# Performance work log

Measured on AMD Instinct MI355X. Metric: run time of the kernel, lower is better.

Reference implementation:

```python
import jax, jax.numpy as jnp
import numpy as np

T, HID, H, KV, D = 2048, 2048, 16, 8, 128
EPS = 1e-6
THETA = 10000.0


def setup_inputs() -> dict:
    key = jax.random.key(0)
    ks = jax.random.split(key, 6)
    positions = jnp.arange(T, dtype=jnp.int64 if jax.config.jax_enable_x64 else jnp.int32)
    hidden_states = jax.random.normal(ks[0], (T, HID), dtype=jnp.float32)
    scale = 0.02
    Wq = jax.random.normal(ks[1], (HID, H * 2 * D), dtype=jnp.float32) * scale
    Wk = jax.random.normal(ks[2], (HID, KV * D), dtype=jnp.float32) * scale
    Wv = jax.random.normal(ks[3], (HID, KV * D), dtype=jnp.float32) * scale
    Wo = jax.random.normal(ks[4], (H * D, HID), dtype=jnp.float32) * scale
    q_norm_w = jnp.zeros((D,), dtype=jnp.float32)  # torch init: zeros, applied as (1+w)
    k_norm_w = jnp.zeros((D,), dtype=jnp.float32)
    return {"positions": positions, "hidden_states": hidden_states, "Wq": Wq,
            "Wk": Wk, "Wv": Wv, "Wo": Wo, "q_norm_w": q_norm_w, "k_norm_w": k_norm_w}


def _rms_norm(x, w):
    # fp32 RMSNorm with (1 + weight) scaling, per last dim
    xf = x.astype(jnp.float32)
    inv = jax.lax.rsqrt(jnp.mean(xf * xf, axis=-1, keepdims=True) + EPS)
    return (xf * inv * (1.0 + w.astype(jnp.float32))).astype(x.dtype)


def _rope(x, positions):
    # neox-style rotary over full head_dim; x: (T, heads, D)
    half = D // 2
    inv_freq = 1.0 / (THETA ** (jnp.arange(0, half, dtype=jnp.float32) / half))
    freqs = positions.astype(jnp.float32)[:, None] * inv_freq  # (T, half)
    cos = jnp.cos(freqs)[:, None, :]  # (T,1,half)
    sin = jnp.sin(freqs)[:, None, :]
    x1, x2 = x[..., :half], x[..., half:]
    return jnp.concatenate([x1 * cos - x2 * sin, x2 * cos + x1 * sin], axis=-1)


def reference(positions, hidden_states, Wq, Wk, Wv, Wo, q_norm_w, k_norm_w):
    scaling = D ** -0.5
    qg = (hidden_states @ Wq).reshape(T, H, 2 * D)
    q, gate = qg[..., :D], qg[..., D:]              # (T,H,D) each
    k = (hidden_states @ Wk).reshape(T, KV, D)
    v = (hidden_states @ Wv).reshape(T, KV, D)
    q = _rms_norm(q, q_norm_w)
    k = _rms_norm(k, k_norm_w)
    q = _rope(q, positions)
    k = _rope(k, positions)
    # GQA: repeat kv heads
    rep = H // KV
    k = jnp.repeat(k, rep, axis=1)                   # (T,H,D)
    v = jnp.repeat(v, rep, axis=1)
    scores = jnp.einsum('thd,shd->hts', q, k) * scaling  # (H,T,T)
    causal = positions[:, None] >= positions[None, :]     # (T,T)
    scores = jnp.where(causal[None], scores, jnp.finfo(scores.dtype).min)
    probs = jax.nn.softmax(scores, axis=-1)
    o = jnp.einsum('hts,shd->thd', probs, v).reshape(T, H * D)
    o = o * jax.nn.sigmoid(gate.reshape(T, H * D))
    return o @ Wo
```

## Files before the change

kernel.cpp:

```cpp
#include <hip/hip_runtime.h>
#include <stdint.h>
#include <math.h>

#define T_SEQ 2048
#define HID   2048
#define NH    16
#define NKV   8
#define DH    128

typedef __bf16 bf16x8 __attribute__((ext_vector_type(8)));
typedef float  f32x4  __attribute__((ext_vector_type(4)));

__device__ __forceinline__ ushort f2bf(float f) {
  uint32_t u = __float_as_uint(f);
  u += 0x7FFF + ((u >> 16) & 1);
  return (ushort)(u >> 16);
}
__device__ __forceinline__ ushort f2bf_rz(float f) {
  return (ushort)(__float_as_uint(f) >> 16);
}
__device__ __forceinline__ float bf2f(ushort u) {
  return __uint_as_float(((uint32_t)u) << 16);
}
__device__ __forceinline__ void gld16(const void* g, void* l) {
  __builtin_amdgcn_global_load_lds(
      (const __attribute__((address_space(1))) uint32_t*)g,
      (__attribute__((address_space(3))) uint32_t*)l, 16, 0, 0);
}

__global__ __launch_bounds__(256) void prep_kernel(
    const float* __restrict__ hs, const float* __restrict__ Wq,
    const float* __restrict__ Wk, const float* __restrict__ Wv,
    const float* __restrict__ Wo, ushort* __restrict__ hs16,
    ushort* __restrict__ Wqt, ushort* __restrict__ Wkt,
    ushort* __restrict__ Wvt, ushort* __restrict__ Wot) {
  int bid = blockIdx.x;
  if (bid < 4096) {
    int i = (bid * 256 + threadIdx.x) * 4;
    float4 v = *(const float4*)(hs + i);
    ushort4 o = {f2bf(v.x), f2bf(v.y), f2bf(v.z), f2bf(v.w)};
    *(ushort4*)(hs16 + i) = o;
    return;
  }
  bid -= 4096;
  const float* src; ushort* dst; int N, bi, bj;
  if (bid < 2048)      { src = Wq; dst = Wqt; N = 4096; bj = bid & 63; bi = bid >> 6; }
  else if (bid < 2560) { bid -= 2048; src = Wk; dst = Wkt; N = 1024; bj = bid & 15; bi = bid >> 4; }
  else if (bid < 3072) { bid -= 2560; src = Wv; dst = Wvt; N = 1024; bj = bid & 15; bi = bid >> 4; }
  else                 { bid -= 3072; src = Wo; dst = Wot; N = 2048; bj = bid & 31; bi = bid >> 5; }
  __shared__ float tile[64][65];
  const int r = threadIdx.x >> 2, cg = (threadIdx.x & 3) * 16;
  const float* sp = src + (size_t)(bi * 64 + r) * N + bj * 64 + cg;
#pragma unroll
  for (int p = 0; p < 4; ++p) {
    float4 v = *(const float4*)(sp + p * 4);
    tile[r][cg + p * 4 + 0] = v.x; tile[r][cg + p * 4 + 1] = v.y;
    tile[r][cg + p * 4 + 2] = v.z; tile[r][cg + p * 4 + 3] = v.w;
  }
  __syncthreads();
  ushort* dp = dst + (size_t)(bj * 64 + r) * HID + bi * 64 + cg;
#pragma unroll
  for (int p = 0; p < 2; ++p) {
    union { uint4 v; ushort u[8]; } o;
#pragma unroll
    for (int j = 0; j < 8; ++j) o.u[j] = f2bf(tile[cg + p * 8 + j][r]);
    *(uint4*)(dp + p * 8) = o.v;
  }
}

template <int MI>
__device__ __forceinline__ void gemm_loop(
    const ushort* __restrict__ A, const ushort* __restrict__ Bt,
    int K, int m0, int n0, ushort* As, ushort* Bs, f32x4 (*acc)[4]) {
  const int tid = threadIdx.x, lane = tid & 63, w = tid >> 6;
  const int quad = lane >> 4, l15 = lane & 15;
  const int wm = (w >> 1) * (MI * 16), wn = (w & 1) * 64;
  const int srow = tid >> 2, sch = tid & 3;
  for (int k0 = 0; k0 < K; k0 += 32) {
    __syncthreads();
#pragma unroll
    for (int p = 0; p < MI / 2; ++p) {
      int row = p * 64 + srow;
      int gch = sch ^ ((row >> 1) & 3);
      gld16(A + (size_t)(m0 + row) * K + k0 + gch * 8,
            As + (p * 256 + w * 64) * 8);
    }
#pragma unroll
    for (int p = 0; p < 2; ++p) {
      int row = p * 64 + srow;
      int gch = sch ^ ((row >> 1) & 3);
      gld16(Bt + (size_t)(n0 + row) * K + k0 + gch * 8,
            Bs + (p * 256 + w * 64) * 8);
    }
    __syncthreads();
    bf16x8 af[MI], bfr[4];
#pragma unroll
    for (int mi = 0; mi < MI; ++mi) {
      int row = wm + mi * 16 + l15;
      int pch = quad ^ ((row >> 1) & 3);
      af[mi] = *(const bf16x8*)(As + row * 32 + pch * 8);
    }
#pragma unroll
    for (int ni = 0; ni < 4; ++ni) {
      int row = wn + ni * 16 + l15;
      int pch = quad ^ ((row >> 1) & 3);
      bfr[ni] = *(const bf16x8*)(Bs + row * 32 + pch * 8);
    }
#pragma unroll
    for (int mi = 0; mi < MI; ++mi)
#pragma unroll
      for (int ni = 0; ni < 4; ++ni)
        acc[mi][ni] = __builtin_amdgcn_mfma_f32_16x16x32_bf16(
            af[mi], bfr[ni], acc[mi][ni], 0, 0, 0);
  }
}

__device__ __forceinline__ void bf16_store(f32x4 (*acc)[4],
                                           ushort* __restrict__ Cb, int Ncols,
                                           int m0, int n0) {
  const int lane = threadIdx.x & 63, w = threadIdx.x >> 6;
  const int quad = lane >> 4, l15 = lane & 15;
  const int wm = (w >> 1) * 64, wn = (w & 1) * 64;
#pragma unroll
  for (int mi = 0; mi < 4; ++mi)
#pragma unroll
    for (int ni = 0; ni < 4; ++ni)
#pragma unroll
      for (int r = 0; r < 4; ++r) {
        int row = m0 + wm + mi * 16 + quad * 4 + r;
        int col = n0 + wn + ni * 16 + l15;
        Cb[(size_t)row * Ncols + col] = f2bf(acc[mi][ni][r]);
      }
}

__global__ __launch_bounds__(256) void gemm_qkv(
    const ushort* __restrict__ hs16, const ushort* __restrict__ Wqt,
    const ushort* __restrict__ Wkt, const ushort* __restrict__ Wvt,
    ushort* __restrict__ q16, ushort* __restrict__ gate16,
    ushort* __restrict__ k16, ushort* __restrict__ v16t) {
  __shared__ ushort As[128 * 32];
  __shared__ ushort Bs[128 * 32];
  f32x4 acc[4][4];
#pragma unroll
  for (int i = 0; i < 4; ++i)
#pragma unroll
    for (int j = 0; j < 4; ++j) acc[i][j] = (f32x4){0.f, 0.f, 0.f, 0.f};
  const int b = blockIdx.x;
  if (b < 512) {
    int mt = b >> 5, nt = b & 31, m0 = mt * 128;
    gemm_loop<4>(hs16, Wqt, HID, m0, nt * 128, As, Bs, acc);
    ushort* dst = ((nt & 1) == 0) ? q16 : gate16;
    bf16_store(acc, dst, NH * DH, m0, (nt >> 1) * 128);
  } else if (b < 640) {
    int f = b - 512, m0 = (f >> 3) * 128, n0 = (f & 7) * 128;
    gemm_loop<4>(hs16, Wkt, HID, m0, n0, As, Bs, acc);
    bf16_store(acc, k16, 1024, m0, n0);
  } else {
    int f = b - 640, m0 = (f >> 4) * 128, n0 = (f & 15) * 128;
    gemm_loop<4>(Wvt, hs16, HID, m0, n0, As, Bs, acc);
    bf16_store(acc, v16t, T_SEQ, m0, n0);
  }
}

__global__ __launch_bounds__(256) void gemm_out(
    const ushort* __restrict__ ob16, const ushort* __restrict__ Wot,
    float* __restrict__ out) {
  __shared__ ushort As[64 * 32];
  __shared__ ushort Bs[128 * 32];
  f32x4 acc[2][4];
#pragma unroll
  for (int i = 0; i < 2; ++i)
#pragma unroll
    for (int j = 0; j < 4; ++j) acc[i][j] = (f32x4){0.f, 0.f, 0.f, 0.f};
  const int b = blockIdx.x;
  const int m0 = (b >> 4) * 64, n0 = (b & 15) * 128;
  gemm_loop<2>(ob16, Wot, HID, m0, n0, As, Bs, acc);
  const int lane = threadIdx.x & 63, w = threadIdx.x >> 6;
  const int quad = lane >> 4, l15 = lane & 15;
  const int wm = (w >> 1) * 32, wn = (w & 1) * 64;
#pragma unroll
  for (int mi = 0; mi < 2; ++mi)
#pragma unroll
    for (int ni = 0; ni < 4; ++ni)
#pragma unroll
      for (int r = 0; r < 4; ++r) {
        int row = m0 + wm + mi * 16 + quad * 4 + r;
        int col = n0 + wn + ni * 16 + l15;
        out[(size_t)row * HID + col] = acc[mi][ni][r];
      }
}

__global__ __launch_bounds__(256) void norm_rope_fast(
    ushort* __restrict__ q16, ushort* __restrict__ k16,
    const int* __restrict__ positions, const float* __restrict__ qw,
    const float* __restrict__ kw) {
  const int tid = threadIdx.x, lg = tid & 15;
  const int r = blockIdx.x * 16 + (tid >> 4);
  ushort* x; const float* wgt; int t;
  if (r < T_SEQ * NH) { t = r >> 4; x = q16 + (size_t)r * DH; wgt = qw; }
  else { int rr = r - T_SEQ * NH; t = rr >> 3; x = k16 + (size_t)rr * DH; wgt = kw; }

  ushort* xp = x + lg * 8;
  ushort4 a = *(const ushort4*)(xp);
  ushort4 bq = *(const ushort4*)(xp + 4);
  float xv[8] = {bf2f(a.x), bf2f(a.y), bf2f(a.z), bf2f(a.w),
                 bf2f(bq.x), bf2f(bq.y), bf2f(bq.z), bf2f(bq.w)};

  float ss = 0.f;
#pragma unroll
  for (int j = 0; j < 8; ++j) ss += xv[j] * xv[j];
  ss += __shfl_xor(ss, 1, 16);
  ss += __shfl_xor(ss, 2, 16);
  ss += __shfl_xor(ss, 4, 16);
  ss += __shfl_xor(ss, 8, 16);
  const float rstd = rsqrtf(ss * (1.f / 128.f) + 1e-6f);

  const int dbase = lg * 8;
  float xn[8];
#pragma unroll
  for (int j = 0; j < 8; ++j) xn[j] = xv[j] * rstd * (1.f + wgt[dbase + j]);

  float pr[8];
#pragma unroll
  for (int j = 0; j < 8; ++j) pr[j] = __shfl_xor(xn[j], 8, 16);

  const float pos = (float)positions[t];
  const int dh = dbase & 63;
  const bool lo = (lg < 8);
  ushort o[8];
#pragma unroll
  for (int j = 0; j < 8; ++j) {
    float rev = pos * exp2f((float)(dh + j) * -0.20762050593045233f) *
                0.15915494309189535f;
    float fr = rev - floorf(rev);
    float s = __builtin_amdgcn_sinf(fr);
    float c = __builtin_amdgcn_cosf(fr);
    float out = lo ? (xn[j] * c - pr[j] * s) : (xn[j] * c + pr[j] * s);
    o[j] = f2bf(out);
  }
  *(ushort4*)(xp)     = (ushort4){o[0], o[1], o[2], o[3]};
  *(ushort4*)(xp + 4) = (ushort4){o[4], o[5], o[6], o[7]};
}

__device__ __forceinline__ void stage_kv(const ushort* __restrict__ k16,
                                         const ushort* __restrict__ v16t,
                                         int kvh, int kt0, ushort* Ksb,
                                         ushort* Vsb, int tid) {
  const int w = tid >> 6;
#pragma unroll
  for (int p = 0; p < 4; ++p) {
    int row = p * 16 + (tid >> 4), ch = tid & 15;
    int gch = ch ^ (row & 15);
    gld16(k16 + ((size_t)(kt0 + row) * NKV + kvh) * DH + gch * 8,
          Ksb + (p * 256 + w * 64) * 8);
  }
#pragma unroll
  for (int p = 0; p < 4; ++p) {
    int row = p * 32 + (tid >> 3), ch = tid & 7;
    int gch = ch ^ (row & 7);
    gld16(v16t + (size_t)(kvh * DH + row) * T_SEQ + kt0 + gch * 8,
          Vsb + (p * 256 + w * 64) * 8);
  }
}

__global__ __launch_bounds__(256) void attn_mfma(
    const ushort* __restrict__ q16, const ushort* __restrict__ k16,
    const ushort* __restrict__ v16t, const float* __restrict__ qnw,
    const float* __restrict__ knw, ushort* __restrict__ Op0,
    ushort* __restrict__ Op1, float* __restrict__ lpart) {
  const int pb = blockIdx.x, h = blockIdx.y, s = blockIdx.z, kvh = h >> 1;
  const int tid = threadIdx.x, lane = tid & 63, w = tid >> 6;
  const int quad = lane >> 4, l15 = lane & 15;

  __shared__ ushort Ks[2][64 * 128];
  __shared__ ushort Vs[2][128 * 64];
  __shared__ ushort Ones[16 * 64];
  __shared__ ushort Ps[4][16][72];

  for (int i = tid; i < 16 * 64; i += 256)
    Ones[i] = (i < 64) ? (ushort)0x3F80 : (ushort)0;

  __shared__ float s8[8];
  __shared__ float bshare;
  {
    float mq = 0.f, mk = 0.f;
    if (tid < 128) { mq = fabsf(1.f + qnw[tid]); mk = fabsf(1.f + knw[tid]); }
#pragma unroll
    for (int off = 32; off >= 1; off >>= 1) {
      mq = fmaxf(mq, __shfl_xor(mq, off, 64));
      mk = fmaxf(mk, __shfl_xor(mk, off, 64));
    }
    if (lane == 0) { s8[w * 2] = mq; s8[w * 2 + 1] = mk; }
    __syncthreads();
    if (tid == 0) {
      float MQ = fmaxf(s8[0], s8[2]), MK = fmaxf(s8[1], s8[3]);
      bshare = 16.3217f * MQ * MK * 1.02f + 0.1f;
    }
    __syncthreads();
  }
  const float B = bshare;
  const float CSC = 0.08838834764831845f * 1.44269504088896f;

#pragma unroll 1
  for (int sel = 0; sel < 2; ++sel) {
    const int qt = sel ? (31 - pb) : pb;
    const int q0 = qt * 64;
    const int ntl = (qt >= s) ? ((qt - s) / 2 + 1) : 0;

    bf16x8 qf[4];
    const ushort* qbase = q16 + ((size_t)(q0 + w * 16 + l15) * NH + h) * DH;
#pragma unroll
    for (int ks = 0; ks < 4; ++ks)
      qf[ks] = *(const bf16x8*)(qbase + ks * 32 + quad * 8);

    f32x4 oacc[9];
#pragma unroll
    for (int i = 0; i < 9; ++i) oacc[i] = (f32x4){0.f, 0.f, 0.f, 0.f};

    if (ntl > 0) stage_kv(k16, v16t, kvh, s * 64, Ks[0], Vs[0], tid);

#pragma unroll 1
    for (int it = 0; it < ntl; ++it) {
      const int kt = s + 2 * it;
      const int kt0 = kt * 64;
      const int cur = it & 1;
      if (it + 1 < ntl) {
        stage_kv(k16, v16t, kvh, (kt + 2) * 64, Ks[cur ^ 1], Vs[cur ^ 1], tid);
        asm volatile("s_waitcnt vmcnt(8)" ::: "memory");
      } else {
        asm volatile("s_waitcnt vmcnt(0)" ::: "memory");
      }
      asm volatile("s_barrier" ::: "memory");

      f32x4 sacc[4];
#pragma unroll
      for (int ni = 0; ni < 4; ++ni) sacc[ni] = (f32x4){0.f, 0.f, 0.f, 0.f};
#pragma unroll
      for (int ks = 0; ks < 4; ++ks)
#pragma unroll
        for (int ni = 0; ni < 4; ++ni) {
          int row = ni * 16 + l15;
          int pch = (ks * 4 + quad) ^ (row & 15);
          bf16x8 kf = *(const bf16x8*)(&Ks[cur][row * 128 + pch * 8]);
          sacc[ni] = __builtin_amdgcn_mfma_f32_16x16x32_bf16(
              qf[ks], kf, sacc[ni], 0, 0, 0);
        }

      const bool diag = (kt == qt);
#pragma unroll
      for (int ni = 0; ni < 4; ++ni) {
        int key = kt0 + ni * 16 + l15;
#pragma unroll
        for (int r = 0; r < 4; ++r) {
          float arg = fmaf(sacc[ni][r], CSC, -B);
          float pv;
          if (diag) {
            int q = q0 + w * 16 + quad * 4 + r;
            pv = (key <= q) ? exp2f(arg) : 0.f;
          } else {
            pv = exp2f(arg);
          }
          Ps[w][quad * 4 + r][ni * 16 + l15] = f2bf_rz(pv);
        }
      }

#pragma unroll
      for (int ks2 = 0; ks2 < 2; ++ks2) {
        bf16x8 pf = *(const bf16x8*)(&Ps[w][l15][ks2 * 32 + quad * 8]);
#pragma unroll
        for (int ni = 0; ni < 9; ++ni) {
          int row = ni * 16 + l15;
          int pch = (ks2 * 4 + quad) ^ (row & 7);
          const ushort* vp = (ni < 8) ? &Vs[cur][row * 64 + pch * 8]
                                      : &Ones[l15 * 64 + pch * 8];
          bf16x8 vf = *(const bf16x8*)(vp);
          oacc[ni] = __builtin_amdgcn_mfma_f32_16x16x32_bf16(
              pf, vf, oacc[ni], 0, 0, 0);
        }
      }
      asm volatile("s_barrier" ::: "memory");
    }

    ushort* Op = s ? Op1 : Op0;
#pragma unroll
    for (int ni = 0; ni < 8; ++ni) {
      int d = ni * 16 + l15;
#pragma unroll
      for (int r = 0; r < 4; ++r) {
        int q = q0 + w * 16 + quad * 4 + r;
        Op[((size_t)h * T_SEQ + q) * DH + d] = f2bf(oacc[ni][r]);
      }
    }
    if (l15 == 0) {
#pragma unroll
      for (int r = 0; r < 4; ++r) {
        int q = q0 + w * 16 + quad * 4 + r;
        lpart[(size_t)s * (NH * T_SEQ) + h * T_SEQ + q] = oacc[8][r];
      }
    }
  }
}

__global__ __launch_bounds__(256) void combine_kernel(
    const ushort* __restrict__ Op0, const ushort* __restrict__ Op1,
    const float* __restrict__ lpart, const ushort* __restrict__ gate16,
    ushort* __restrict__ ob16) {
  const int t = blockIdx.x, tid = threadIdx.x;
  const int h = tid >> 4, d0 = (tid & 15) * 8;
  const int NT = NH * T_SEQ;
  const float l = lpart[h * T_SEQ + t] + lpart[NT + h * T_SEQ + t];
  const float inv = 1.0f / l;
  const size_t po = ((size_t)h * T_SEQ + t) * DH + d0;
  ushort4 a0 = *(const ushort4*)(Op0 + po);
  ushort4 a1 = *(const ushort4*)(Op0 + po + 4);
  ushort4 b0 = *(const ushort4*)(Op1 + po);
  ushort4 b1 = *(const ushort4*)(Op1 + po + 4);
  const ushort* gp = gate16 + (size_t)t * (NH * DH) + h * DH + d0;
  ushort4 g0 = *(const ushort4*)(gp);
  ushort4 g1 = *(const ushort4*)(gp + 4);
  float oa[8] = {bf2f(a0.x), bf2f(a0.y), bf2f(a0.z), bf2f(a0.w),
                 bf2f(a1.x), bf2f(a1.y), bf2f(a1.z), bf2f(a1.w)};
  float ob[8] = {bf2f(b0.x), bf2f(b0.y), bf2f(b0.z), bf2f(b0.w),
                 bf2f(b1.x), bf2f(b1.y), bf2f(b1.z), bf2f(b1.w)};
  float gg[8] = {bf2f(g0.x), bf2f(g0.y), bf2f(g0.z), bf2f(g0.w),
                 bf2f(g1.x), bf2f(g1.y), bf2f(g1.z), bf2f(g1.w)};
  ushort r[8];
#pragma unroll
  for (int i = 0; i < 8; ++i) {
    float o = (oa[i] + ob[i]) * inv;
    o = o / (1.0f + exp2f(-gg[i] * 1.44269504088896f));
    r[i] = f2bf(o);
  }
  ushort* op = ob16 + (size_t)t * (NH * DH) + h * DH + d0;
  *(ushort4*)(op)     = (ushort4){r[0], r[1], r[2], r[3]};
  *(ushort4*)(op + 4) = (ushort4){r[4], r[5], r[6], r[7]};
}

extern "C" void kernel_launch(void* const* d_in, const int* in_sizes, int n_in,
                              void* d_out, int out_size, void* d_ws, size_t ws_size,
                              hipStream_t stream) {
  const int*   positions = (const int*)d_in[0];
  const float* hs  = (const float*)d_in[1];
  const float* Wq  = (const float*)d_in[2];
  const float* Wk  = (const float*)d_in[3];
  const float* Wv  = (const float*)d_in[4];
  const float* Wo  = (const float*)d_in[5];
  const float* qnw = (const float*)d_in[6];
  const float* knw = (const float*)d_in[7];
  float* out = (float*)d_out;

  const size_t MB = 1 << 20;
  uint8_t* ws = (uint8_t*)d_ws;
  ushort* hs16  = (ushort*)(ws + 0);
  ushort* Op0   = (ushort*)(ws + 0);
  ushort* Wqt   = (ushort*)(ws + 8 * MB);
  ushort* Op1   = (ushort*)(ws + 8 * MB);
  ushort* Wkt   = (ushort*)(ws + 24 * MB);
  ushort* ob16  = (ushort*)(ws + 24 * MB);
  ushort* Wvt   = (ushort*)(ws + 28 * MB);
  ushort* v16t  = (ushort*)(ws + 32 * MB);
  ushort* k16   = (ushort*)(ws + 36 * MB);
  ushort* q16   = (ushort*)(ws + 40 * MB);
  ushort* gate16= (ushort*)(ws + 48 * MB);
  ushort* Wot   = (ushort*)(ws + 56 * MB);
  float*  lpart = (float*)d_out;

  prep_kernel<<<8192, 256, 0, stream>>>(hs, Wq, Wk, Wv, Wo,
                                        hs16, Wqt, Wkt, Wvt, Wot);
  gemm_qkv<<<768, 256, 0, stream>>>(hs16, Wqt, Wkt, Wvt,
                                    q16, gate16, k16, v16t);
  norm_rope_fast<<<3072, 256, 0, stream>>>(q16, k16, positions, qnw, knw);
  attn_mfma<<<dim3(16, NH, 2), 256, 0, stream>>>(q16, k16, v16t, qnw, knw,
                                                 Op0, Op1, lpart);
  combine_kernel<<<T_SEQ, 256, 0, stream>>>(Op0, Op1, lpart, gate16, ob16);
  gemm_out<<<512, 256, 0, stream>>>(ob16, Wot, out);
}
```

Baseline: 272.4 us.

## Fuse attention combine into attn kernel; split-K output GEMM with atomics

Attention no longer splits the key range into two partial passes. Each block now processes every causal key tile for its query tiles and applies normalisation and the sigmoid gate directly in its epilogue, which removes the combine kernel and the partial-output round trip through memory. The output projection switches to 128x128 tiles with a 2-way K split and accumulates into a pre-zeroed output using float atomics, keeping the grid at 512 blocks. The cost is half as many attention blocks, so less parallelism there, plus an extra zeroing kernel, atomic traffic, and a summation order that is no longer deterministic.

Result: slower. 312.2 us (+14.6%).

```diff
diff --git a/kernel.cpp b/kernel.cpp
--- a/kernel.cpp
+++ b/kernel.cpp
@@ -26,6 +26,11 @@
   __builtin_amdgcn_global_load_lds(
       (const __attribute__((address_space(1))) uint32_t*)g,
       (__attribute__((address_space(3))) uint32_t*)l, 16, 0, 0);
+}
+
+__global__ __launch_bounds__(256) void zero_out(float* __restrict__ out) {
+  int i = (blockIdx.x * 256 + threadIdx.x) * 4;
+  *(float4*)(out + i) = (float4){0.f, 0.f, 0.f, 0.f};
 }
 
 __global__ __launch_bounds__(256) void prep_kernel(
@@ -71,25 +76,26 @@
 template <int MI>
 __device__ __forceinline__ void gemm_loop(
     const ushort* __restrict__ A, const ushort* __restrict__ Bt,
-    int K, int m0, int n0, ushort* As, ushort* Bs, f32x4 (*acc)[4]) {
+    int ld, int kbeg, int kend, int m0, int n0, ushort* As, ushort* Bs,
+    f32x4 (*acc)[4]) {
   const int tid = threadIdx.x, lane = tid & 63, w = tid >> 6;
   const int quad = lane >> 4, l15 = lane & 15;
   const int wm = (w >> 1) * (MI * 16), wn = (w & 1) * 64;
   const int srow = tid >> 2, sch = tid & 3;
-  for (int k0 = 0; k0 < K; k0 += 32) {
+  for (int k0 = kbeg; k0 < kend; k0 += 32) {
     __syncthreads();
 #pragma unroll
     for (int p = 0; p < MI / 2; ++p) {
       int row = p * 64 + srow;
       int gch = sch ^ ((row >> 1) & 3);
-      gld16(A + (size_t)(m0 + row) * K + k0 + gch * 8,
+      gld16(A + (size_t)(m0 + row) * ld + k0 + gch * 8,
             As + (p * 256 + w * 64) * 8);
     }
 #pragma unroll
     for (int p = 0; p < 2; ++p) {
       int row = p * 64 + srow;
       int gch = sch ^ ((row >> 1) & 3);
-      gld16(Bt + (size_t)(n0 + row) * K + k0 + gch * 8,
+      gld16(Bt + (size_t)(n0 + row) * ld + k0 + gch * 8,
             Bs + (p * 256 + w * 64) * 8);
     }
     __syncthreads();
@@ -148,16 +154,16 @@
   const int b = blockIdx.x;
   if (b < 512) {
     int mt = b >> 5, nt = b & 31, m0 = mt * 128;
-    gemm_loop<4>(hs16, Wqt, HID, m0, nt * 128, As, Bs, acc);
+    gemm_loop<4>(hs16, Wqt, HID, 0, HID, m0, nt * 128, As, Bs, acc);
     ushort* dst = ((nt & 1) == 0) ? q16 : gate16;
     bf16_store(acc, dst, NH * DH, m0, (nt >> 1) * 128);
   } else if (b < 640) {
     int f = b - 512, m0 = (f >> 3) * 128, n0 = (f & 7) * 128;
-    gemm_loop<4>(hs16, Wkt, HID, m0, n0, As, Bs, acc);
+    gemm_loop<4>(hs16, Wkt, HID, 0, HID, m0, n0, As, Bs, acc);
     bf16_store(acc, k16, 1024, m0, n0);
   } else {
     int f = b - 640, m0 = (f >> 4) * 128, n0 = (f & 15) * 128;
-    gemm_loop<4>(Wvt, hs16, HID, m0, n0, As, Bs, acc);
+    gemm_loop<4>(Wvt, hs16, HID, 0, HID, m0, n0, As, Bs, acc);
     bf16_store(acc, v16t, T_SEQ, m0, n0);
   }
 }
@@ -165,28 +171,32 @@
 __global__ __launch_bounds__(256) void gemm_out(
     const ushort* __restrict__ ob16, const ushort* __restrict__ Wot,
     float* __restrict__ out) {
-  __shared__ ushort As[64 * 32];
+  __shared__ ushort As[128 * 32];
   __shared__ ushort Bs[128 * 32];
-  f32x4 acc[2][4];
-#pragma unroll
-  for (int i = 0; i < 2; ++i)
+  f32x4 acc[4][4];
+#pragma unroll
+  for (int i = 0; i < 4; ++i)
 #pragma unroll
     for (int j = 0; j < 4; ++j) acc[i][j] = (f32x4){0.f, 0.f, 0.f, 0.f};
   const int b = blockIdx.x;
-  const int m0 = (b >> 4) * 64, n0 = (b & 15) * 128;
-  gemm_loop<2>(ob16, Wot, HID, m0, n0, As, Bs, acc);
+  const int tilei = b & 255, ks = b >> 8;
+  const int m0 = (tilei >> 4) * 128, n0 = (tilei & 15) * 128;
+  const int kbeg = ks * (HID / 2);
+  gemm_loop<4>(ob16, Wot, HID, kbeg, kbeg + HID / 2, m0, n0, As, Bs, acc);
   const int lane = threadIdx.x & 63, w = threadIdx.x >> 6;
   const int quad = lane >> 4, l15 = lane & 15;
-  const int wm = (w >> 1) * 32, wn = (w & 1) * 64;
-#pragma unroll
-  for (int mi = 0; mi < 2; ++mi)
+  const int wm = (w >> 1) * 64, wn = (w & 1) * 64;
+#pragma unroll
+  for (int mi = 0; mi < 4; ++mi)
 #pragma unroll
     for (int ni = 0; ni < 4; ++ni)
 #pragma unroll
       for (int r = 0; r < 4; ++r) {
         int row = m0 + wm + mi * 16 + quad * 4 + r;
         int col = n0 + wn + ni * 16 + l15;
-        out[(size_t)row * HID + col] = acc[mi][ni][r];
+        __hip_atomic_fetch_add(&out[(size_t)row * HID + col],
+                               acc[mi][ni][r], __ATOMIC_RELAXED,
+                               __HIP_MEMORY_SCOPE_AGENT);
       }
 }
 
@@ -266,9 +276,9 @@
 __global__ __launch_bounds__(256) void attn_mfma(
     const ushort* __restrict__ q16, const ushort* __restrict__ k16,
     const ushort* __restrict__ v16t, const float* __restrict__ qnw,
-    const float* __restrict__ knw, ushort* __restrict__ Op0,
-    ushort* __restrict__ Op1, float* __restrict__ lpart) {
-  const int pb = blockIdx.x, h = blockIdx.y, s = blockIdx.z, kvh = h >> 1;
+    const float* __restrict__ knw, const ushort* __restrict__ gate16,
+    ushort* __restrict__ ob16) {
+  const int pb = blockIdx.x, h = blockIdx.y, kvh = h >> 1;
   const int tid = threadIdx.x, lane = tid & 63, w = tid >> 6;
   const int quad = lane >> 4, l15 = lane & 15;
 
@@ -305,7 +315,7 @@
   for (int sel = 0; sel < 2; ++sel) {
     const int qt = sel ? (31 - pb) : pb;
     const int q0 = qt * 64;
-    const int ntl = (qt >= s) ? ((qt - s) / 2 + 1) : 0;
+    const int ntl = qt + 1;
 
     bf16x8 qf[4];
     const ushort* qbase = q16 + ((size_t)(q0 + w * 16 + l15) * NH + h) * DH;
@@ -317,15 +327,14 @@
 #pragma unroll
     for (int i = 0; i < 9; ++i) oacc[i] = (f32x4){0.f, 0.f, 0.f, 0.f};
 
-    if (ntl > 0) stage_kv(k16, v16t, kvh, s * 64, Ks[0], Vs[0], tid);
+    stage_kv(k16, v16t, kvh, 0, Ks[0], Vs[0], tid);
 
 #pragma unroll 1
     for (int it = 0; it < ntl; ++it) {
-      const int kt = s + 2 * it;
-      const int kt0 = kt * 64;
+      const int kt0 = it * 64;
       const int cur = it & 1;
       if (it + 1 < ntl) {
-        stage_kv(k16, v16t, kvh, (kt + 2) * 64, Ks[cur ^ 1], Vs[cur ^ 1], tid);
+        stage_kv(k16, v16t, kvh, (it + 1) * 64, Ks[cur ^ 1], Vs[cur ^ 1], tid);
         asm volatile("s_waitcnt vmcnt(8)" ::: "memory");
       } else {
         asm volatile("s_waitcnt vmcnt(0)" ::: "memory");
@@ -346,7 +355,7 @@
               qf[ks], kf, sacc[ni], 0, 0, 0);
         }
 
-      const bool diag = (kt == qt);
+      const bool diag = (it == qt);
 #pragma unroll
       for (int ni = 0; ni < 4; ++ni) {
         int key = kt0 + ni * 16 + l15;
@@ -381,59 +390,23 @@
       asm volatile("s_barrier" ::: "memory");
     }
 
-    ushort* Op = s ? Op1 : Op0;
-#pragma unroll
-    for (int ni = 0; ni < 8; ++ni) {
-      int d = ni * 16 + l15;
-#pragma unroll
-      for (int r = 0; r < 4; ++r) {
-        int q = q0 + w * 16 + quad * 4 + r;
-        Op[((size_t)h * T_SEQ + q) * DH + d] = f2bf(oacc[ni][r]);
-      }
-    }
-    if (l15 == 0) {
-#pragma unroll
-      for (int r = 0; r < 4; ++r) {
-        int q = q0 + w * 16 + quad * 4 + r;
-        lpart[(size_t)s * (NH * T_SEQ) + h * T_SEQ + q] = oacc[8][r];
-      }
-    }
-  }
-}
-
-__global__ __launch_bounds__(256) void combine_kernel(
-    const ushort* __restrict__ Op0, const ushort* __restrict__ Op1,
-    const float* __restrict__ lpart, const ushort* __restrict__ gate16,
-    ushort* __restrict__ ob16) {
-  const int t = blockIdx.x, tid = threadIdx.x;
-  const int h = tid >> 4, d0 = (tid & 15) * 8;
-  const int NT = NH * T_SEQ;
-  const float l = lpart[h * T_SEQ + t] + lpart[NT + h * T_SEQ + t];
-  const float inv = 1.0f / l;
-  const size_t po = ((size_t)h * T_SEQ + t) * DH + d0;
-  ushort4 a0 = *(const ushort4*)(Op0 + po);
-  ushort4 a1 = *(const ushort4*)(Op0 + po + 4);
-  ushort4 b0 = *(const ushort4*)(Op1 + po);
-  ushort4 b1 = *(const ushort4*)(Op1 + po + 4);
-  const ushort* gp = gate16 + (size_t)t * (NH * DH) + h * DH + d0;
-  ushort4 g0 = *(const ushort4*)(gp);
-  ushort4 g1 = *(const ushort4*)(gp + 4);
-  float oa[8] = {bf2f(a0.x), bf2f(a0.y), bf2f(a0.z), bf2f(a0.w),
-                 bf2f(a1.x), bf2f(a1.y), bf2f(a1.z), bf2f(a1.w)};
-  float ob[8] = {bf2f(b0.x), bf2f(b0.y), bf2f(b0.z), bf2f(b0.w),
-                 bf2f(b1.x), bf2f(b1.y), bf2f(b1.z), bf2f(b1.w)};
-  float gg[8] = {bf2f(g0.x), bf2f(g0.y), bf2f(g0.z), bf2f(g0.w),
-                 bf2f(g1.x), bf2f(g1.y), bf2f(g1.z), bf2f(g1.w)};
-  ushort r[8];
-#pragma unroll
-  for (int i = 0; i < 8; ++i) {
-    float o = (oa[i] + ob[i]) * inv;
-    o = o / (1.0f + exp2f(-gg[i] * 1.44269504088896f));
-    r[i] = f2bf(o);
-  }
-  ushort* op = ob16 + (size_t)t * (NH * DH) + h * DH + d0;
-  *(ushort4*)(op)     = (ushort4){r[0], r[1], r[2], r[3]};
-  *(ushort4*)(op + 4) = (ushort4){r[4], r[5], r[6], r[7]};
+#pragma unroll
+    for (int r = 0; r < 4; ++r) {
+      float l = __shfl(oacc[8][r], quad << 4, 64);
+      float inv = 1.0f / l;
+      const int q = q0 + w * 16 + quad * 4 + r;
+      const ushort* gp = gate16 + (size_t)q * (NH * DH) + h * DH;
+      ushort* op = ob16 + (size_t)q * (NH * DH) + h * DH;
+#pragma unroll
+      for (int ni = 0; ni < 8; ++ni) {
+        int d = ni * 16 + l15;
+        float g = bf2f(gp[d]);
+        float o = oacc[ni][r] * inv;
+        o = o / (1.0f + exp2f(-g * 1.44269504088896f));
+        op[d] = f2bf(o);
+      }
+    }
+  }
 }
 
 extern "C" void kernel_launch(void* const* d_in, const int* in_sizes, int n_in,
@@ -452,9 +425,7 @@
   const size_t MB = 1 << 20;
   uint8_t* ws = (uint8_t*)d_ws;
   ushort* hs16  = (ushort*)(ws + 0);
-  ushort* Op0   = (ushort*)(ws + 0);
   ushort* Wqt   = (ushort*)(ws + 8 * MB);
-  ushort* Op1   = (ushort*)(ws + 8 * MB);
   ushort* Wkt   = (ushort*)(ws + 24 * MB);
   ushort* ob16  = (ushort*)(ws + 24 * MB);
   ushort* Wvt   = (ushort*)(ws + 28 * MB);
@@ -463,15 +434,14 @@
   ushort* q16   = (ushort*)(ws + 40 * MB);
   ushort* gate16= (ushort*)(ws + 48 * MB);
   ushort* Wot   = (ushort*)(ws + 56 * MB);
-  float*  lpart = (float*)d_out;
-
+
+  zero_out<<<4096, 256, 0, stream>>>(out);
   prep_kernel<<<8192, 256, 0, stream>>>(hs, Wq, Wk, Wv, Wo,
                                         hs16, Wqt, Wkt, Wvt, Wot);
   gemm_qkv<<<768, 256, 0, stream>>>(hs16, Wqt, Wkt, Wvt,
                                     q16, gate16, k16, v16t);
   norm_rope_fast<<<3072, 256, 0, stream>>>(q16, k16, positions, qnw, knw);
-  attn_mfma<<<dim3(16, NH, 2), 256, 0, stream>>>(q16, k16, v16t, qnw, knw,
-                                                 Op0, Op1, lpart);
-  combine_kernel<<<T_SEQ, 256, 0, stream>>>(Op0, Op1, lpart, gate16, ob16);
+  attn_mfma<<<dim3(16, NH), 256, 0, stream>>>(q16, k16, v16t, qnw, knw,
+                                              gate16, ob16);
   gemm_out<<<512, 256, 0, stream>>>(ob16, Wot, out);
 }
```
